# Kernel tuning notes

Hardware: AMD Instinct MI355X
Metric: run time of the kernel (lower is better)

The kernel has to match this reference:

```python
import jax, jax.numpy as jnp
import numpy as np

N, E = 50000, 800000
IN, HID, OUT = 128, 128, 64
H, ED = 4, 3
D = HID // H  # per-head dim = 32


def _w(key, shape):
    fan_in = shape[-1]
    return jax.random.normal(key, shape, dtype=jnp.float32) / np.sqrt(fan_in)


def setup_inputs() -> dict:
    key = jax.random.key(0)
    ks = jax.random.split(key, 32)
    inp = {
        "x": jax.random.normal(ks[0], (N, IN), dtype=jnp.float32),
        "edge_index": jax.random.randint(ks[1], (2, E), 0, N, dtype=jnp.int32),
        "edge_attr": jax.random.normal(ks[2], (E, ED), dtype=jnp.float32),
        # layer 1 TransformerConv (bias=False)
        "Wq1": _w(ks[3], (HID, IN)), "Wk1": _w(ks[4], (HID, IN)),
        "Wv1": _w(ks[5], (HID, IN)), "We1": _w(ks[6], (HID, ED)),
        "Ws1": _w(ks[7], (HID, IN)),
        # layer 1 MLP [HID,HID,HID]
        "M1a": _w(ks[8], (HID, HID)), "b1a": jnp.zeros((HID,), jnp.float32),
        "M1b": _w(ks[9], (HID, HID)), "b1b": jnp.zeros((HID,), jnp.float32),
        # layer 2 TransformerConv
        "Wq2": _w(ks[10], (HID, HID)), "Wk2": _w(ks[11], (HID, HID)),
        "Wv2": _w(ks[12], (HID, HID)), "We2": _w(ks[13], (HID, ED)),
        "Ws2": _w(ks[14], (HID, HID)),
        # layer 2 MLP
        "M2a": _w(ks[15], (HID, HID)), "b2a": jnp.zeros((HID,), jnp.float32),
        "M2b": _w(ks[16], (HID, HID)), "b2b": jnp.zeros((HID,), jnp.float32),
        # final MLP [HID,HID,OUT], plain_last=False
        "Wf1": _w(ks[17], (HID, HID)), "bf1": jnp.zeros((HID,), jnp.float32),
        "Wf2": _w(ks[18], (OUT, HID)), "bf2": jnp.zeros((OUT,), jnp.float32),
    }
    return inp


def _gelu(x):
    return jax.nn.gelu(x, approximate=True)


def _transformer_conv(x, src, dst, edge_attr, Wq, Wk, Wv, We, Ws, n_nodes):
    # PyG TransformerConv: x_j = x[src] (message source), x_i = x[dst] (target)
    q = (x @ Wq.T).reshape(n_nodes, H, D)
    e = (edge_attr @ We.T).reshape(-1, H, D)              # [E,H,D]
    k = (x @ Wk.T).reshape(n_nodes, H, D)[src] + e        # [E,H,D]
    v = (x @ Wv.T).reshape(n_nodes, H, D)[src] + e        # [E,H,D]
    alpha = jnp.einsum("ehd,ehd->eh", q[dst], k) / jnp.float32(np.sqrt(D))
    # segment softmax over incoming edges of each target node
    m = jax.ops.segment_max(alpha, dst, num_segments=n_nodes)  # [N,H]
    m = jnp.where(jnp.isfinite(m), m, 0.0)
    p = jnp.exp(alpha - m[dst])
    s = jax.ops.segment_sum(p, dst, num_segments=n_nodes)      # [N,H]
    a = p / jnp.maximum(s[dst], 1e-16)                         # [E,H]
    out = jax.ops.segment_sum(a[:, :, None] * v, dst, num_segments=n_nodes)
    out = out.reshape(n_nodes, H * D)
    # root_weight=True (default): skip connection through lin_skip (no bias)
    return out + x @ Ws.T


def _mlp2(x, Wa, ba, Wb, bb):
    # PyG MLP with plain_last=False: act after every linear, norm=None
    h = _gelu(x @ Wa.T + ba)
    return _gelu(h @ Wb.T + bb)


def reference(x, edge_index, edge_attr,
              Wq1, Wk1, Wv1, We1, Ws1, M1a, b1a, M1b, b1b,
              Wq2, Wk2, Wv2, We2, Ws2, M2a, b2a, M2b, b2b,
              Wf1, bf1, Wf2, bf2):
    n_nodes = x.shape[0]
    src, dst = edge_index[0], edge_index[1]
    h = _transformer_conv(x, src, dst, edge_attr, Wq1, Wk1, Wv1, We1, Ws1, n_nodes)
    h = h + _mlp2(h, M1a, b1a, M1b, b1b)
    h = _transformer_conv(h, src, dst, edge_attr, Wq2, Wk2, Wv2, We2, Ws2, n_nodes)
    h = h + _mlp2(h, M2a, b2a, M2b, b2b)
    return _mlp2(h, Wf1, bf1, Wf2, bf2)
```

## Files before the change

### kernel.cpp

```cpp
#include <hip/hip_runtime.h>
#include <hip/hip_bf16.h>
#include <math.h>

#define NN 50000
#define NE 800000
#define NPAD 50048
#define NB_SCAN 196

typedef unsigned short u16;
typedef unsigned int u32;
typedef __attribute__((ext_vector_type(8))) short short8;
typedef __attribute__((ext_vector_type(4))) float float4v;

__device__ __forceinline__ float us2f(u16 u) { return __uint_as_float(((unsigned)u) << 16); }
__device__ __forceinline__ float blo(u32 u) { return __uint_as_float(u << 16); }
__device__ __forceinline__ float bhi(u32 u) { return __uint_as_float(u & 0xffff0000u); }
__device__ __forceinline__ u16 f2us(float f) {
    unsigned x = __float_as_uint(f);
    return (u16)((x + 0x7FFFu + ((x >> 16) & 1u)) >> 16);
}
__device__ __forceinline__ float gelu_f(float x) {
    float p = x * x;
    float t = x * fmaf(p, 0.0713548162726f, 1.5957691216057308f);
    float e = __expf(-t);
    return x * __builtin_amdgcn_rcpf(1.0f + e);
}
__device__ __forceinline__ void lds_fence() {
    asm volatile("s_waitcnt lgkmcnt(0)" ::: "memory");
}

__device__ __forceinline__ float4v mfma4p(const u16* __restrict__ WP, int tile, int l,
                                          short8 a0, short8 a1, short8 a2, short8 a3) {
    const short8* wp = (const short8*)WP + (size_t)tile * 256 + l;
    short8 b0 = wp[0], b1 = wp[64], b2 = wp[128], b3 = wp[192];
    float4v acc = {0.f, 0.f, 0.f, 0.f};
    acc = __builtin_amdgcn_mfma_f32_16x16x32_bf16(a0, b0, acc, 0, 0, 0);
    acc = __builtin_amdgcn_mfma_f32_16x16x32_bf16(a1, b1, acc, 0, 0, 0);
    acc = __builtin_amdgcn_mfma_f32_16x16x32_bf16(a2, b2, acc, 0, 0, 0);
    acc = __builtin_amdgcn_mfma_f32_16x16x32_bf16(a3, b3, acc, 0, 0, 0);
    return acc;
}


__global__ void k_hist(const int* __restrict__ dstv, int* __restrict__ deg) {
    int e = blockIdx.x * blockDim.x + threadIdx.x;
    if (e < NE) atomicAdd(&deg[dstv[e]], 1);
}

__global__ __launch_bounds__(256) void k_scan1(const int* __restrict__ deg,
                                               int* __restrict__ rowstart,
                                               int* __restrict__ bsum) {
    __shared__ int wtot[4];
    int i = blockIdx.x * 256 + threadIdx.x;
    int lane = threadIdx.x & 63, w = threadIdx.x >> 6;
    int v = (i < NN) ? deg[i] : 0;
    int incl = v;
#pragma unroll
    for (int d = 1; d < 64; d <<= 1) {
        int tv = __shfl_up(incl, d);
        if (lane >= d) incl += tv;
    }
    if (lane == 63) wtot[w] = incl;
    __syncthreads();
    if (threadIdx.x == 0) {
        int s = 0;
#pragma unroll
        for (int j = 0; j < 4; ++j) { int t = wtot[j]; wtot[j] = s; s += t; }
        bsum[blockIdx.x] = s;
    }
    __syncthreads();
    if (i < NN) rowstart[i] = incl - v + wtot[w];
}

__global__ __launch_bounds__(256) void k_scan2(int* __restrict__ bsum) {
    __shared__ int wtot[4];
    int t = threadIdx.x;
    int lane = t & 63, w = t >> 6;
    int v = (t < NB_SCAN) ? bsum[t] : 0;
    int incl = v;
#pragma unroll
    for (int d = 1; d < 64; d <<= 1) {
        int tv = __shfl_up(incl, d);
        if (lane >= d) incl += tv;
    }
    if (lane == 63) wtot[w] = incl;
    __syncthreads();
    if (t == 0) {
        int s = 0;
#pragma unroll
        for (int j = 0; j < 4; ++j) { int tt = wtot[j]; wtot[j] = s; s += tt; }
    }
    __syncthreads();
    if (t < NB_SCAN) bsum[t] = incl - v + wtot[w];
}

__global__ void k_scan3(const int* __restrict__ bsum, int* __restrict__ rowstart,
                        int* __restrict__ cursor) {
    int i = blockIdx.x * 256 + threadIdx.x;
    if (i < NN) {
        int v = rowstart[i] + bsum[blockIdx.x];
        rowstart[i] = v;
        cursor[i] = v;
    }
    if (i == 0) rowstart[NN] = NE;
}

__global__ void k_scatter(const int* __restrict__ srcv, const int* __restrict__ dstv,
                          const float* __restrict__ eattr, int* __restrict__ cursor,
                          int4* __restrict__ rec) {
    int e = blockIdx.x * blockDim.x + threadIdx.x;
    if (e >= NE) return;
    int dst = dstv[e];
    int pos = atomicAdd(&cursor[dst], 1);
    int4 r;
    r.x = srcv[e];
    r.y = __float_as_int(eattr[e * 3 + 0]);
    r.z = __float_as_int(eattr[e * 3 + 1]);
    r.w = __float_as_int(eattr[e * 3 + 2]);
    rec[pos] = r;
}


struct CvtEnt { const float* s; u16* d; int n; };
struct CvtTab { CvtEnt e[14]; };
__global__ void k_cvt_w(CvtTab tab) {
    CvtEnt E = tab.e[blockIdx.x >> 3];
    int chunk = blockIdx.x & 7;
    int per = E.n >> 3;
    int lo = chunk * per, hi = lo + per;
    for (int o = lo + threadIdx.x; o < hi; o += blockDim.x) {
        int tile = o >> 11;
        int q = (o >> 9) & 3;
        int l = (o >> 3) & 63;
        int j = o & 7;
        int row = tile * 16 + (l & 15);
        int col = q * 32 + (l >> 4) * 8 + j;
        E.d[o] = f2us(E.s[row * 128 + col]);
    }
}

__global__ void k_prep_we(const float* __restrict__ We1, const float* __restrict__ We2,
                          float4* __restrict__ WeP1, float4* __restrict__ WeP2) {
    int t = threadIdx.x;
    if (t < 128) {
        WeP1[t] = make_float4(We1[t * 3], We1[t * 3 + 1], We1[t * 3 + 2], 0.f);
    } else {
        int c = t - 128;
        WeP2[c] = make_float4(We2[c * 3], We2[c * 3 + 1], We2[c * 3 + 2], 0.f);
    }
}


__device__ __forceinline__ void stage_plain(u16* buf, int kb, int m, int tt, float4v acc) {
#pragma unroll
    for (int r = 0; r < 4; ++r) buf[(kb * 4 + r) * 136 + tt * 16 + m] = f2us(acc[r]);
}
__device__ __forceinline__ void store128(const u16* buf, u16* dst, int r0w, int coff, int l) {
#pragma unroll
    for (int it = 0; it < 4; ++it) {
        int j = it * 64 + l;
        int row = j >> 4, col = (j & 15) * 8;
        *(uint4*)(dst + (size_t)(r0w + row) * 512 + coff + col) = *(const uint4*)&buf[row * 136 + col];
    }
}
__device__ __forceinline__ void read_frags(const u16* buf, int m, int kb,
                                           short8& f0, short8& f1, short8& f2, short8& f3) {
    const u16* p = buf + m * 136 + kb * 8;
    f0 = *(const short8*)(p);
    f1 = *(const short8*)(p + 32);
    f2 = *(const short8*)(p + 64);
    f3 = *(const short8*)(p + 96);
}

__device__ __forceinline__ void compute_g(const u16* buf, const float4* __restrict__ WeP,
                                          float4* __restrict__ G, int r0w, int m, int kb) {
    const u16* qr = buf + m * 136 + kb * 32;
    short8 qv0 = *(const short8*)(qr);
    short8 qv1 = *(const short8*)(qr + 8);
    short8 qv2 = *(const short8*)(qr + 16);
    short8 qv3 = *(const short8*)(qr + 24);
    const float4* wp = WeP + kb * 32;
    float g0 = 0.f, g1 = 0.f, g2 = 0.f;
    const short8* qs[4] = {&qv0, &qv1, &qv2, &qv3};
#pragma unroll
    for (int b = 0; b < 4; ++b) {
        const u16* qq = (const u16*)qs[b];
#pragma unroll
        for (int d = 0; d < 8; ++d) {
            float qvf = us2f(qq[d]);
            float4 wv = wp[b * 8 + d];
            g0 = fmaf(qvf, wv.x, g0);
            g1 = fmaf(qvf, wv.y, g1);
            g2 = fmaf(qvf, wv.z, g2);
        }
    }
    G[(size_t)(r0w + m) * 4 + kb] = make_float4(g0, g1, g2, 0.f);
}



__global__ __launch_bounds__(64, 4) void k_qkvs1(const float* __restrict__ Ain,
                                                 const u16* __restrict__ W,
                                                 const float4* __restrict__ WeP,
                                                 float4* __restrict__ G,
                                                 u16* __restrict__ QKVS) {
    __shared__ u16 my[16 * 136];
    int l = threadIdx.x;
    int m = l & 15, kb = l >> 4;
    int r0w = blockIdx.x * 16;

    short8 a0, a1, a2, a3;
    {
        const float* ap = Ain + (size_t)(r0w + m) * 128;
        bool ok = (r0w + m) < NN;
        short8* dsts[4] = {&a0, &a1, &a2, &a3};
#pragma unroll
        for (int i = 0; i < 4; ++i) {
            short8 r;
            if (ok) {
                const float* p = ap + (kb + i * 4) * 8;
                float4 f0 = *(const float4*)p;
                float4 f1 = *(const float4*)(p + 4);
                r[0]=(short)f2us(f0.x); r[1]=(short)f2us(f0.y); r[2]=(short)f2us(f0.z); r[3]=(short)f2us(f0.w);
                r[4]=(short)f2us(f1.x); r[5]=(short)f2us(f1.y); r[6]=(short)f2us(f1.z); r[7]=(short)f2us(f1.w);
            } else {
#pragma unroll
                for (int j = 0; j < 8; ++j) r[j] = 0;
            }
            *dsts[i] = r;
        }
    }

#pragma unroll
    for (int tt = 0; tt < 8; ++tt) stage_plain(my, kb, m, tt, mfma4p(W, tt, l, a0, a1, a2, a3));
    lds_fence();
    store128(my, QKVS, r0w, 0, l);
    compute_g(my, WeP, G, r0w, m, kb);
    lds_fence();
#pragma unroll
    for (int tt = 0; tt < 4; ++tt) {
        float4v acc = mfma4p(W, 8 + tt, l, a0, a1, a2, a3);
        int c = tt * 32 + 8 * (m >> 2) + (m & 3);
#pragma unroll
        for (int r = 0; r < 4; ++r) my[(kb * 4 + r) * 136 + c] = f2us(acc[r]);
    }
#pragma unroll
    for (int tt = 0; tt < 4; ++tt) {
        float4v acc = mfma4p(W, 16 + tt, l, a0, a1, a2, a3);
        int c = tt * 32 + 8 * (m >> 2) + (m & 3) + 4;
#pragma unroll
        for (int r = 0; r < 4; ++r) my[(kb * 4 + r) * 136 + c] = f2us(acc[r]);
    }
    lds_fence();
    store128(my, QKVS, r0w, 128, l);
    lds_fence();
#pragma unroll
    for (int tt = 0; tt < 4; ++tt) {
        float4v acc = mfma4p(W, 12 + tt, l, a0, a1, a2, a3);
        int c = tt * 32 + 8 * (m >> 2) + (m & 3);
#pragma unroll
        for (int r = 0; r < 4; ++r) my[(kb * 4 + r) * 136 + c] = f2us(acc[r]);
    }
#pragma unroll
    for (int tt = 0; tt < 4; ++tt) {
        float4v acc = mfma4p(W, 20 + tt, l, a0, a1, a2, a3);
        int c = tt * 32 + 8 * (m >> 2) + (m & 3) + 4;
#pragma unroll
        for (int r = 0; r < 4; ++r) my[(kb * 4 + r) * 136 + c] = f2us(acc[r]);
    }
    lds_fence();
    store128(my, QKVS, r0w, 256, l);
    lds_fence();
#pragma unroll
    for (int tt = 0; tt < 8; ++tt) stage_plain(my, kb, m, tt, mfma4p(W, 24 + tt, l, a0, a1, a2, a3));
    lds_fence();
    store128(my, QKVS, r0w, 384, l);
}


__global__ __launch_bounds__(64, 4) void k_mlp_qkvs(const u16* __restrict__ Ain,
                                                    const u16* __restrict__ Wm,
                                                    const float* __restrict__ bias1,
                                                    const float* __restrict__ bias2,
                                                    const u16* __restrict__ Wq,
                                                    const float4* __restrict__ WeP,
                                                    float4* __restrict__ G,
                                                    u16* __restrict__ QKVS) {
    __shared__ u16 sh[16 * 136];
    __shared__ u16 t1[16 * 136];
    int l = threadIdx.x;
    int m = l & 15, kb = l >> 4;
    int r0w = blockIdx.x * 16;

    const short8* arow = (const short8*)(Ain + (size_t)(r0w + m) * 128);
    short8 a0 = arow[kb], a1 = arow[kb + 4], a2 = arow[kb + 8], a3 = arow[kb + 12];
    {
        u16* p = sh + m * 136 + kb * 8;
        *(short8*)(p) = a0;
        *(short8*)(p + 32) = a1;
        *(short8*)(p + 64) = a2;
        *(short8*)(p + 96) = a3;
    }
#pragma unroll
    for (int tt = 0; tt < 8; ++tt) {
        float4v acc = mfma4p(Wm, tt, l, a0, a1, a2, a3);
        float bv = bias1[tt * 16 + m];
#pragma unroll
        for (int r = 0; r < 4; ++r)
            t1[(kb * 4 + r) * 136 + tt * 16 + m] = f2us(gelu_f(acc[r] + bv));
    }
    lds_fence();
    short8 c0, c1, c2, c3;
    read_frags(t1, m, kb, c0, c1, c2, c3);
#pragma unroll
    for (int tt = 0; tt < 8; ++tt) {
        float4v acc = mfma4p(Wm + 16384, tt, l, c0, c1, c2, c3);
        float bv = bias2[tt * 16 + m];
#pragma unroll
        for (int r = 0; r < 4; ++r) {
            int idx = (kb * 4 + r) * 136 + tt * 16 + m;
            sh[idx] = f2us(gelu_f(acc[r] + bv) + us2f(sh[idx]));
        }
    }
    lds_fence();
    short8 h0, h1, h2, h3;
    read_frags(sh, m, kb, h0, h1, h2, h3);

#pragma unroll
    for (int tt = 0; tt < 8; ++tt) stage_plain(t1, kb, m, tt, mfma4p(Wq, tt, l, h0, h1, h2, h3));
    lds_fence();
    store128(t1, QKVS, r0w, 0, l);
    compute_g(t1, WeP, G, r0w, m, kb);
    lds_fence();
#pragma unroll
    for (int tt = 0; tt < 4; ++tt) {
        float4v acc = mfma4p(Wq, 8 + tt, l, h0, h1, h2, h3);
        int c = tt * 32 + 8 * (m >> 2) + (m & 3);
#pragma unroll
        for (int r = 0; r < 4; ++r) t1[(kb * 4 + r) * 136 + c] = f2us(acc[r]);
    }
#pragma unroll
    for (int tt = 0; tt < 4; ++tt) {
        float4v acc = mfma4p(Wq, 16 + tt, l, h0, h1, h2, h3);
        int c = tt * 32 + 8 * (m >> 2) + (m & 3) + 4;
#pragma unroll
        for (int r = 0; r < 4; ++r) t1[(kb * 4 + r) * 136 + c] = f2us(acc[r]);
    }
    lds_fence();
    store128(t1, QKVS, r0w, 128, l);
    lds_fence();
#pragma unroll
    for (int tt = 0; tt < 4; ++tt) {
        float4v acc = mfma4p(Wq, 12 + tt, l, h0, h1, h2, h3);
        int c = tt * 32 + 8 * (m >> 2) + (m & 3);
#pragma unroll
        for (int r = 0; r < 4; ++r) t1[(kb * 4 + r) * 136 + c] = f2us(acc[r]);
    }
#pragma unroll
    for (int tt = 0; tt < 4; ++tt) {
        float4v acc = mfma4p(Wq, 20 + tt, l, h0, h1, h2, h3);
        int c = tt * 32 + 8 * (m >> 2) + (m & 3) + 4;
#pragma unroll
        for (int r = 0; r < 4; ++r) t1[(kb * 4 + r) * 136 + c] = f2us(acc[r]);
    }
    lds_fence();
    store128(t1, QKVS, r0w, 256, l);
    lds_fence();
#pragma unroll
    for (int tt = 0; tt < 8; ++tt) stage_plain(t1, kb, m, tt, mfma4p(Wq, 24 + tt, l, h0, h1, h2, h3));
    lds_fence();
    store128(t1, QKVS, r0w, 384, l);
}


__global__ __launch_bounds__(64, 4) void k_mlp_final(const u16* __restrict__ Ain,
                                                     const u16* __restrict__ Wm,
                                                     const float* __restrict__ bias1,
                                                     const float* __restrict__ bias2,
                                                     const u16* __restrict__ Wf,
                                                     const float* __restrict__ bf1,
                                                     const float* __restrict__ bf2,
                                                     float* __restrict__ outp) {
    __shared__ u16 sh[16 * 136];
    __shared__ u16 t1[16 * 136];
    int l = threadIdx.x;
    int m = l & 15, kb = l >> 4;
    int r0w = blockIdx.x * 16;

    const short8* arow = (const short8*)(Ain + (size_t)(r0w + m) * 128);
    short8 a0 = arow[kb], a1 = arow[kb + 4], a2 = arow[kb + 8], a3 = arow[kb + 12];
    {
        u16* p = sh + m * 136 + kb * 8;
        *(short8*)(p) = a0;
        *(short8*)(p + 32) = a1;
        *(short8*)(p + 64) = a2;
        *(short8*)(p + 96) = a3;
    }
#pragma unroll
    for (int tt = 0; tt < 8; ++tt) {
        float4v acc = mfma4p(Wm, tt, l, a0, a1, a2, a3);
        float bv = bias1[tt * 16 + m];
#pragma unroll
        for (int r = 0; r < 4; ++r)
            t1[(kb * 4 + r) * 136 + tt * 16 + m] = f2us(gelu_f(acc[r] + bv));
    }
    lds_fence();
    short8 c0, c1, c2, c3;
    read_frags(t1, m, kb, c0, c1, c2, c3);
#pragma unroll
    for (int tt = 0; tt < 8; ++tt) {
        float4v acc = mfma4p(Wm + 16384, tt, l, c0, c1, c2, c3);
        float bv = bias2[tt * 16 + m];
#pragma unroll
        for (int r = 0; r < 4; ++r) {
            int idx = (kb * 4 + r) * 136 + tt * 16 + m;
            sh[idx] = f2us(gelu_f(acc[r] + bv) + us2f(sh[idx]));
        }
    }
    lds_fence();
    short8 h0, h1, h2, h3;
    read_frags(sh, m, kb, h0, h1, h2, h3);
#pragma unroll
    for (int tt = 0; tt < 8; ++tt) {
        float4v acc = mfma4p(Wf, tt, l, h0, h1, h2, h3);
        float bv = bf1[tt * 16 + m];
#pragma unroll
        for (int r = 0; r < 4; ++r)
            t1[(kb * 4 + r) * 136 + tt * 16 + m] = f2us(gelu_f(acc[r] + bv));
    }
    lds_fence();
    short8 f0, f1, f2, f3;
    read_frags(t1, m, kb, f0, f1, f2, f3);
    lds_fence();
#pragma unroll
    for (int tt = 0; tt < 4; ++tt) {
        float4v acc = mfma4p(Wf + 16384, tt, l, f0, f1, f2, f3);
        float bv = bf2[tt * 16 + m];
#pragma unroll
        for (int r = 0; r < 4; ++r)
            t1[(kb * 4 + r) * 136 + tt * 16 + m] = f2us(gelu_f(acc[r] + bv));
    }
    lds_fence();
#pragma unroll
    for (int it = 0; it < 2; ++it) {
        int j = it * 64 + l;
        int row = j >> 3, col = (j & 7) * 8;
        int grow = r0w + row;
        if (grow < NN) {
            uint4 pk = *(const uint4*)&t1[row * 136 + col];
            const u16* pv = (const u16*)&pk;
            float* po = outp + (size_t)grow * 64 + col;
            float4 o0 = {us2f(pv[0]), us2f(pv[1]), us2f(pv[2]), us2f(pv[3])};
            float4 o1 = {us2f(pv[4]), us2f(pv[5]), us2f(pv[6]), us2f(pv[7])};
            *(float4*)po = o0;
            *(float4*)(po + 4) = o1;
        }
    }
}


__global__ __launch_bounds__(256) void k_conv(const int* __restrict__ rowstart,
                                              const int4* __restrict__ rec,
                                              const u16* __restrict__ qkvs,
                                              const float4* __restrict__ WeP,
                                              const float4* __restrict__ G,
                                              u16* __restrict__ out) {
    int n = blockIdx.x * 4 + (threadIdx.x >> 6);
    int l = threadIdx.x & 63;
    int quarter = l >> 4;
    int li = l & 15;
    int c0 = li * 8;
    const u16* qrow = qkvs + (size_t)n * 512;
    uint4 qu = *(const uint4*)(qrow + c0);
    const float SC = 0.17677669529663687f;
    float q0 = blo(qu.x) * SC, q1 = bhi(qu.x) * SC, q2 = blo(qu.y) * SC, q3 = bhi(qu.y) * SC;
    float q4 = blo(qu.z) * SC, q5 = bhi(qu.z) * SC, q6 = blo(qu.w) * SC, q7 = bhi(qu.w) * SC;
    float4 gg = G[(size_t)n * 4 + (li >> 2)];
    float g0 = gg.x * SC, g1 = gg.y * SC, g2 = gg.z * SC;

    int e0 = rowstart[n], e1 = rowstart[n + 1];
    int deg = e1 - e0;
    float ss = 0.f, S0 = 0.f, S1 = 0.f, S2 = 0.f;
    float o0 = 0.f, o1 = 0.f, o2 = 0.f, o3 = 0.f, o4 = 0.f, o5 = 0.f, o6 = 0.f, o7 = 0.f;

    if (deg > 0) {
        int iters = (deg + 3) >> 2;
        int eb = e0 + quarter;
        int elast = e1 - 1;
        int4 r0 = rec[min(eb, elast)];
        int4 r1 = rec[min(eb + 4, elast)];
        const u16* kvB = qkvs + 128 + (size_t)li * 16;
        uint4 kA = *(const uint4*)(kvB + (size_t)r0.x * 512);
        uint4 kB = *(const uint4*)(kvB + (size_t)r0.x * 512 + 8);
        for (int i = 0; i < iters; ++i) {
            int4 r2 = rec[min(eb + 4 * (i + 2), elast)];
            const u16* kp = kvB + (size_t)r1.x * 512;
            uint4 nA = *(const uint4*)(kp);
            uint4 nB = *(const uint4*)(kp + 8);
            float part = q0 * blo(kA.x) + q1 * bhi(kA.x) + q2 * blo(kA.y) + q3 * bhi(kA.y)
                       + q4 * blo(kB.x) + q5 * bhi(kB.x) + q6 * blo(kB.y) + q7 * bhi(kB.y);
            part += __shfl_xor(part, 1);
            part += __shfl_xor(part, 2);
            float ea0 = __int_as_float(r0.y), ea1 = __int_as_float(r0.z), ea2 = __int_as_float(r0.w);
            float alpha = fmaf(ea2, g2, fmaf(ea1, g1, fmaf(ea0, g0, part)));
            float p = __expf(fminf(alpha, 80.f));
            p = (eb + 4 * i < e1) ? p : 0.f;
            o0 = fmaf(p, blo(kA.z), o0);
            o1 = fmaf(p, bhi(kA.z), o1);
            o2 = fmaf(p, blo(kA.w), o2);
            o3 = fmaf(p, bhi(kA.w), o3);
            o4 = fmaf(p, blo(kB.z), o4);
            o5 = fmaf(p, bhi(kB.z), o5);
            o6 = fmaf(p, blo(kB.w), o6);
            o7 = fmaf(p, bhi(kB.w), o7);
            ss += p;
            S0 = fmaf(p, ea0, S0);
            S1 = fmaf(p, ea1, S1);
            S2 = fmaf(p, ea2, S2);
            r0 = r1; r1 = r2; kA = nA; kB = nB;
        }
    }
    o0 += __shfl_xor(o0, 16); o1 += __shfl_xor(o1, 16); o2 += __shfl_xor(o2, 16); o3 += __shfl_xor(o3, 16);
    o4 += __shfl_xor(o4, 16); o5 += __shfl_xor(o5, 16); o6 += __shfl_xor(o6, 16); o7 += __shfl_xor(o7, 16);
    ss += __shfl_xor(ss, 16); S0 += __shfl_xor(S0, 16); S1 += __shfl_xor(S1, 16); S2 += __shfl_xor(S2, 16);
    o0 += __shfl_xor(o0, 32); o1 += __shfl_xor(o1, 32); o2 += __shfl_xor(o2, 32); o3 += __shfl_xor(o3, 32);
    o4 += __shfl_xor(o4, 32); o5 += __shfl_xor(o5, 32); o6 += __shfl_xor(o6, 32); o7 += __shfl_xor(o7, 32);
    ss += __shfl_xor(ss, 32); S0 += __shfl_xor(S0, 32); S1 += __shfl_xor(S1, 32); S2 += __shfl_xor(S2, 32);

    if (quarter == 0) {
        float inv = __builtin_amdgcn_rcpf(fmaxf(ss, 1e-16f));
        float4 w0 = WeP[c0 + 0], w1 = WeP[c0 + 1], w2 = WeP[c0 + 2], w3 = WeP[c0 + 3];
        float4 w4 = WeP[c0 + 4], w5 = WeP[c0 + 5], w6 = WeP[c0 + 6], w7 = WeP[c0 + 7];
        o0 += w0.x * S0 + w0.y * S1 + w0.z * S2;
        o1 += w1.x * S0 + w1.y * S1 + w1.z * S2;
        o2 += w2.x * S0 + w2.y * S1 + w2.z * S2;
        o3 += w3.x * S0 + w3.y * S1 + w3.z * S2;
        o4 += w4.x * S0 + w4.y * S1 + w4.z * S2;
        o5 += w5.x * S0 + w5.y * S1 + w5.z * S2;
        o6 += w6.x * S0 + w6.y * S1 + w6.z * S2;
        o7 += w7.x * S0 + w7.y * S1 + w7.z * S2;
        uint4 su = *(const uint4*)(qrow + 384 + c0);
        float r0v = fmaf(o0, inv, blo(su.x));
        float r1v = fmaf(o1, inv, bhi(su.x));
        float r2v = fmaf(o2, inv, blo(su.y));
        float r3v = fmaf(o3, inv, bhi(su.y));
        float r4v = fmaf(o4, inv, blo(su.z));
        float r5v = fmaf(o5, inv, bhi(su.z));
        float r6v = fmaf(o6, inv, blo(su.w));
        float r7v = fmaf(o7, inv, bhi(su.w));
        uint4 ou;
        ou.x = (u32)f2us(r0v) | ((u32)f2us(r1v) << 16);
        ou.y = (u32)f2us(r2v) | ((u32)f2us(r3v) << 16);
        ou.z = (u32)f2us(r4v) | ((u32)f2us(r5v) << 16);
        ou.w = (u32)f2us(r6v) | ((u32)f2us(r7v) << 16);
        *(uint4*)(out + (size_t)n * 128 + c0) = ou;
    }
}


extern "C" void kernel_launch(void* const* d_in, const int* in_sizes, int n_in,
                              void* d_out, int out_size, void* d_ws, size_t ws_size,
                              hipStream_t stream) {
    const float* x = (const float*)d_in[0];
    const int* ei = (const int*)d_in[1];
    const float* eattr = (const float*)d_in[2];
    const float* Wq1 = (const float*)d_in[3];
    const float* Wk1 = (const float*)d_in[4];
    const float* Wv1 = (const float*)d_in[5];
    const float* We1 = (const float*)d_in[6];
    const float* Ws1 = (const float*)d_in[7];
    const float* M1a = (const float*)d_in[8];
    const float* b1a = (const float*)d_in[9];
    const float* M1b = (const float*)d_in[10];
    const float* b1b = (const float*)d_in[11];
    const float* Wq2 = (const float*)d_in[12];
    const float* Wk2 = (const float*)d_in[13];
    const float* Wv2 = (const float*)d_in[14];
    const float* We2 = (const float*)d_in[15];
    const float* Ws2 = (const float*)d_in[16];
    const float* M2a = (const float*)d_in[17];
    const float* b2a = (const float*)d_in[18];
    const float* M2b = (const float*)d_in[19];
    const float* b2b = (const float*)d_in[20];
    const float* Wf1 = (const float*)d_in[21];
    const float* bf1 = (const float*)d_in[22];
    const float* Wf2 = (const float*)d_in[23];
    const float* bf2 = (const float*)d_in[24];

    char* ws = (char*)d_ws;
    size_t off = 0;
    auto alloc = [&](size_t bytes) -> void* {
        void* p = ws + off;
        off = (off + bytes + 255) & ~(size_t)255;
        return p;
    };
    int* deg = (int*)alloc((size_t)NN * 4);
    int* rowstart = (int*)alloc((size_t)(NN + 1) * 4);
    int* cursor = (int*)alloc((size_t)NN * 4);
    int* bsum = (int*)alloc((size_t)NB_SCAN * 4);
    int4* rec = (int4*)alloc((size_t)NE * 16);
    u16* QKVS = (u16*)alloc((size_t)NPAD * 512 * 2);
    u16* Ha = (u16*)alloc((size_t)NPAD * 128 * 2);
    float4* G = (float4*)alloc((size_t)NPAD * 4 * 16);
    float4* WeP1 = (float4*)alloc(128 * 16);
    float4* WeP2 = (float4*)alloc(128 * 16);
    u16* WB[14];
    const int wsz[14] = {16384, 16384, 16384, 16384, 16384, 16384, 16384,
                         16384, 16384, 16384, 16384, 16384, 16384, 8192};
    for (int i = 0; i < 14; ++i) WB[i] = (u16*)alloc((size_t)wsz[i] * 2);

    const int* srcv = ei;
    const int* dstv = ei + NE;

    hipMemsetAsync(deg, 0, (size_t)NN * 4, stream);
    k_hist<<<(NE + 255) / 256, 256, 0, stream>>>(dstv, deg);
    k_scan1<<<NB_SCAN, 256, 0, stream>>>(deg, rowstart, bsum);
    k_scan2<<<1, 256, 0, stream>>>(bsum);
    k_scan3<<<NB_SCAN, 256, 0, stream>>>(bsum, rowstart, cursor);
    k_scatter<<<(NE + 255) / 256, 256, 0, stream>>>(srcv, dstv, eattr, cursor, rec);

    CvtTab tab;
    const float* wsrc[14] = {Wq1, Wk1, Wv1, Ws1, Wq2, Wk2, Wv2, Ws2,
                             M1a, M1b, M2a, M2b, Wf1, Wf2};
    for (int i = 0; i < 14; ++i) { tab.e[i].s = wsrc[i]; tab.e[i].d = WB[i]; tab.e[i].n = wsz[i]; }
    k_cvt_w<<<112, 256, 0, stream>>>(tab);
    k_prep_we<<<1, 256, 0, stream>>>(We1, We2, WeP1, WeP2);

    dim3 gg(NPAD / 16);
    dim3 gconv(NN / 4);

    k_qkvs1<<<gg, 64, 0, stream>>>(x, WB[0], WeP1, G, QKVS);
    k_conv<<<gconv, 256, 0, stream>>>(rowstart, rec, QKVS, WeP1, G, Ha);
    k_mlp_qkvs<<<gg, 64, 0, stream>>>(Ha, WB[8], b1a, b1b, WB[4], WeP2, G, QKVS);
    k_conv<<<gconv, 256, 0, stream>>>(rowstart, rec, QKVS, WeP2, G, Ha);
    k_mlp_final<<<gg, 64, 0, stream>>>(Ha, WB[10], b2a, b2b, WB[12], bf1, bf2, (float*)d_out);
}
```

Measured before the change: 412.1 us.

## Stage weight tiles in LDS shared by four waves per block in GEMM kernels

The three dense node-GEMM kernels now run four 16-row waves per 256-thread block. The waves cooperatively copy each 32 KB weight section into shared memory and then read MFMA B fragments from LDS, where each wave previously read the weights straight from global memory. This cuts global and L2 weight traffic by roughly a factor of four. In exchange it adds many __syncthreads barriers, serialises each load before its compute phase, and uses about 32 KB or more of LDS per block, which may lower occupancy.

Measured after the change: 437.1 us. 6.1% more time.

```diff
diff --git a/kernel.cpp b/kernel.cpp
--- a/kernel.cpp
+++ b/kernel.cpp
@@ -29,9 +29,9 @@
     asm volatile("s_waitcnt lgkmcnt(0)" ::: "memory");
 }
 
-__device__ __forceinline__ float4v mfma4p(const u16* __restrict__ WP, int tile, int l,
+__device__ __forceinline__ float4v mfma4l(const u16* sec, int t, int l,
                                           short8 a0, short8 a1, short8 a2, short8 a3) {
-    const short8* wp = (const short8*)WP + (size_t)tile * 256 + l;
+    const short8* wp = (const short8*)(sec + t * 2048) + l;
     short8 b0 = wp[0], b1 = wp[64], b2 = wp[128], b3 = wp[192];
     float4v acc = {0.f, 0.f, 0.f, 0.f};
     acc = __builtin_amdgcn_mfma_f32_16x16x32_bf16(a0, b0, acc, 0, 0, 0);
@@ -39,6 +39,29 @@
     acc = __builtin_amdgcn_mfma_f32_16x16x32_bf16(a2, b2, acc, 0, 0, 0);
     acc = __builtin_amdgcn_mfma_f32_16x16x32_bf16(a3, b3, acc, 0, 0, 0);
     return acc;
+}
+
+__device__ __forceinline__ void load_sec32(const u16* __restrict__ s0,
+                                           const u16* __restrict__ s1,
+                                           u16* secbuf, int w, int l) {
+    const u16* base = (w < 2) ? s0 : s1;
+    int off = (w & 1) * 8;
+    int dbase = (w < 2) ? 0 : 8192;
+#pragma unroll
+    for (int j = 0; j < 8; ++j) {
+        int ch = off + j;
+        uint4 v = *(const uint4*)(base + ch * 512 + l * 8);
+        *(uint4*)(secbuf + dbase + ch * 512 + l * 8) = v;
+    }
+}
+__device__ __forceinline__ void load_sec16(const u16* __restrict__ s0,
+                                           u16* secbuf, int w, int l) {
+#pragma unroll
+    for (int j = 0; j < 4; ++j) {
+        int ch = w * 4 + j;
+        uint4 v = *(const uint4*)(s0 + ch * 512 + l * 8);
+        *(uint4*)(secbuf + ch * 512 + l * 8) = v;
+    }
 }
 
 
@@ -175,16 +198,12 @@
 __device__ __forceinline__ void compute_g(const u16* buf, const float4* __restrict__ WeP,
                                           float4* __restrict__ G, int r0w, int m, int kb) {
     const u16* qr = buf + m * 136 + kb * 32;
-    short8 qv0 = *(const short8*)(qr);
-    short8 qv1 = *(const short8*)(qr + 8);
-    short8 qv2 = *(const short8*)(qr + 16);
-    short8 qv3 = *(const short8*)(qr + 24);
     const float4* wp = WeP + kb * 32;
     float g0 = 0.f, g1 = 0.f, g2 = 0.f;
-    const short8* qs[4] = {&qv0, &qv1, &qv2, &qv3};
 #pragma unroll
     for (int b = 0; b < 4; ++b) {
-        const u16* qq = (const u16*)qs[b];
+        short8 qv = *(const short8*)(qr + b * 8);
+        const u16* qq = (const u16*)&qv;
 #pragma unroll
         for (int d = 0; d < 8; ++d) {
             float qvf = us2f(qq[d]);
@@ -199,15 +218,17 @@
 
 
 
-__global__ __launch_bounds__(64, 4) void k_qkvs1(const float* __restrict__ Ain,
-                                                 const u16* __restrict__ W,
-                                                 const float4* __restrict__ WeP,
-                                                 float4* __restrict__ G,
-                                                 u16* __restrict__ QKVS) {
-    __shared__ u16 my[16 * 136];
-    int l = threadIdx.x;
-    int m = l & 15, kb = l >> 4;
-    int r0w = blockIdx.x * 16;
+__global__ __launch_bounds__(256) void k_qkvs1(const float* __restrict__ Ain,
+                                               const u16* __restrict__ W,
+                                               const float4* __restrict__ WeP,
+                                               float4* __restrict__ G,
+                                               u16* __restrict__ QKVS) {
+    __shared__ u16 secbuf[8 * 2048];
+    __shared__ u16 myb[4][16 * 136];
+    int tid = threadIdx.x;
+    int l = tid & 63, w = tid >> 6, m = l & 15, kb = l >> 4;
+    int r0w = blockIdx.x * 64 + w * 16;
+    u16* my = myb[w];
 
     short8 a0, a1, a2, a3;
     {
@@ -231,66 +252,77 @@
         }
     }
 
-#pragma unroll
-    for (int tt = 0; tt < 8; ++tt) stage_plain(my, kb, m, tt, mfma4p(W, tt, l, a0, a1, a2, a3));
+    load_sec32(W, W + 8192, secbuf, w, l);
+    __syncthreads();
+#pragma unroll
+    for (int tt = 0; tt < 8; ++tt) stage_plain(my, kb, m, tt, mfma4l(secbuf, tt, l, a0, a1, a2, a3));
     lds_fence();
     store128(my, QKVS, r0w, 0, l);
     compute_g(my, WeP, G, r0w, m, kb);
-    lds_fence();
-#pragma unroll
-    for (int tt = 0; tt < 4; ++tt) {
-        float4v acc = mfma4p(W, 8 + tt, l, a0, a1, a2, a3);
+    __syncthreads();
+    load_sec32(W + 8 * 2048, W + 16 * 2048, secbuf, w, l);
+    __syncthreads();
+#pragma unroll
+    for (int tt = 0; tt < 4; ++tt) {
+        float4v acc = mfma4l(secbuf, tt, l, a0, a1, a2, a3);
         int c = tt * 32 + 8 * (m >> 2) + (m & 3);
 #pragma unroll
         for (int r = 0; r < 4; ++r) my[(kb * 4 + r) * 136 + c] = f2us(acc[r]);
     }
 #pragma unroll
     for (int tt = 0; tt < 4; ++tt) {
-        float4v acc = mfma4p(W, 16 + tt, l, a0, a1, a2, a3);
+        float4v acc = mfma4l(secbuf, 4 + tt, l, a0, a1, a2, a3);
         int c = tt * 32 + 8 * (m >> 2) + (m & 3) + 4;
 #pragma unroll
         for (int r = 0; r < 4; ++r) my[(kb * 4 + r) * 136 + c] = f2us(acc[r]);
     }
     lds_fence();
     store128(my, QKVS, r0w, 128, l);
-    lds_fence();
-#pragma unroll
-    for (int tt = 0; tt < 4; ++tt) {
-        float4v acc = mfma4p(W, 12 + tt, l, a0, a1, a2, a3);
+    __syncthreads();
+    load_sec32(W + 12 * 2048, W + 20 * 2048, secbuf, w, l);
+    __syncthreads();
+#pragma unroll
+    for (int tt = 0; tt < 4; ++tt) {
+        float4v acc = mfma4l(secbuf, tt, l, a0, a1, a2, a3);
         int c = tt * 32 + 8 * (m >> 2) + (m & 3);
 #pragma unroll
         for (int r = 0; r < 4; ++r) my[(kb * 4 + r) * 136 + c] = f2us(acc[r]);
     }
 #pragma unroll
     for (int tt = 0; tt < 4; ++tt) {
-        float4v acc = mfma4p(W, 20 + tt, l, a0, a1, a2, a3);
+        float4v acc = mfma4l(secbuf, 4 + tt, l, a0, a1, a2, a3);
         int c = tt * 32 + 8 * (m >> 2) + (m & 3) + 4;
 #pragma unroll
         for (int r = 0; r < 4; ++r) my[(kb * 4 + r) * 136 + c] = f2us(acc[r]);
     }
     lds_fence();
     store128(my, QKVS, r0w, 256, l);
-    lds_fence();
-#pragma unroll
-    for (int tt = 0; tt < 8; ++tt) stage_plain(my, kb, m, tt, mfma4p(W, 24 + tt, l, a0, a1, a2, a3));
+    __syncthreads();
+    load_sec32(W + 24 * 2048, W + 28 * 2048, secbuf, w, l);
+    __syncthreads();
+#pragma unroll
+    for (int tt = 0; tt < 8; ++tt) stage_plain(my, kb, m, tt, mfma4l(secbuf, tt, l, a0, a1, a2, a3));
     lds_fence();
     store128(my, QKVS, r0w, 384, l);
 }
 
 
-__global__ __launch_bounds__(64, 4) void k_mlp_qkvs(const u16* __restrict__ Ain,
-                                                    const u16* __restrict__ Wm,
-                                                    const float* __restrict__ bias1,
-                                                    const float* __restrict__ bias2,
-                                                    const u16* __restrict__ Wq,
-                                                    const float4* __restrict__ WeP,
-                                                    float4* __restrict__ G,
-                                                    u16* __restrict__ QKVS) {
-    __shared__ u16 sh[16 * 136];
-    __shared__ u16 t1[16 * 136];
-    int l = threadIdx.x;
-    int m = l & 15, kb = l >> 4;
-    int r0w = blockIdx.x * 16;
+__global__ __launch_bounds__(256) void k_mlp_qkvs(const u16* __restrict__ Ain,
+                                                  const u16* __restrict__ Wm,
+                                                  const float* __restrict__ bias1,
+                                                  const float* __restrict__ bias2,
+                                                  const u16* __restrict__ Wq,
+                                                  const float4* __restrict__ WeP,
+                                                  float4* __restrict__ G,
+                                                  u16* __restrict__ QKVS) {
+    __shared__ u16 secbuf[8 * 2048];
+    __shared__ u16 shb[4][16 * 136];
+    __shared__ u16 t1b[4][16 * 136];
+    int tid = threadIdx.x;
+    int l = tid & 63, w = tid >> 6, m = l & 15, kb = l >> 4;
+    int r0w = blockIdx.x * 64 + w * 16;
+    u16* sh = shb[w];
+    u16* t1 = t1b[w];
 
     const short8* arow = (const short8*)(Ain + (size_t)(r0w + m) * 128);
     short8 a0 = arow[kb], a1 = arow[kb + 4], a2 = arow[kb + 8], a3 = arow[kb + 12];
@@ -301,9 +333,11 @@
         *(short8*)(p + 64) = a2;
         *(short8*)(p + 96) = a3;
     }
+    load_sec32(Wm, Wm + 8192, secbuf, w, l);
+    __syncthreads();
 #pragma unroll
     for (int tt = 0; tt < 8; ++tt) {
-        float4v acc = mfma4p(Wm, tt, l, a0, a1, a2, a3);
+        float4v acc = mfma4l(secbuf, tt, l, a0, a1, a2, a3);
         float bv = bias1[tt * 16 + m];
 #pragma unroll
         for (int r = 0; r < 4; ++r)
@@ -312,9 +346,12 @@
     lds_fence();
     short8 c0, c1, c2, c3;
     read_frags(t1, m, kb, c0, c1, c2, c3);
+    __syncthreads();
+    load_sec32(Wm + 16384, Wm + 16384 + 8192, secbuf, w, l);
+    __syncthreads();
 #pragma unroll
     for (int tt = 0; tt < 8; ++tt) {
-        float4v acc = mfma4p(Wm + 16384, tt, l, c0, c1, c2, c3);
+        float4v acc = mfma4l(secbuf, tt, l, c0, c1, c2, c3);
         float bv = bias2[tt * 16 + m];
 #pragma unroll
         for (int r = 0; r < 4; ++r) {
@@ -325,67 +362,78 @@
     lds_fence();
     short8 h0, h1, h2, h3;
     read_frags(sh, m, kb, h0, h1, h2, h3);
-
-#pragma unroll
-    for (int tt = 0; tt < 8; ++tt) stage_plain(t1, kb, m, tt, mfma4p(Wq, tt, l, h0, h1, h2, h3));
+    __syncthreads();
+    load_sec32(Wq, Wq + 8192, secbuf, w, l);
+    __syncthreads();
+#pragma unroll
+    for (int tt = 0; tt < 8; ++tt) stage_plain(t1, kb, m, tt, mfma4l(secbuf, tt, l, h0, h1, h2, h3));
     lds_fence();
     store128(t1, QKVS, r0w, 0, l);
     compute_g(t1, WeP, G, r0w, m, kb);
-    lds_fence();
-#pragma unroll
-    for (int tt = 0; tt < 4; ++tt) {
-        float4v acc = mfma4p(Wq, 8 + tt, l, h0, h1, h2, h3);
+    __syncthreads();
+    load_sec32(Wq + 8 * 2048, Wq + 16 * 2048, secbuf, w, l);
+    __syncthreads();
+#pragma unroll
+    for (int tt = 0; tt < 4; ++tt) {
+        float4v acc = mfma4l(secbuf, tt, l, h0, h1, h2, h3);
         int c = tt * 32 + 8 * (m >> 2) + (m & 3);
 #pragma unroll
         for (int r = 0; r < 4; ++r) t1[(kb * 4 + r) * 136 + c] = f2us(acc[r]);
     }
 #pragma unroll
     for (int tt = 0; tt < 4; ++tt) {
-        float4v acc = mfma4p(Wq, 16 + tt, l, h0, h1, h2, h3);
+        float4v acc = mfma4l(secbuf, 4 + tt, l, h0, h1, h2, h3);
         int c = tt * 32 + 8 * (m >> 2) + (m & 3) + 4;
 #pragma unroll
         for (int r = 0; r < 4; ++r) t1[(kb * 4 + r) * 136 + c] = f2us(acc[r]);
     }
     lds_fence();
     store128(t1, QKVS, r0w, 128, l);
-    lds_fence();
-#pragma unroll
-    for (int tt = 0; tt < 4; ++tt) {
-        float4v acc = mfma4p(Wq, 12 + tt, l, h0, h1, h2, h3);
+    __syncthreads();
+    load_sec32(Wq + 12 * 2048, Wq + 20 * 2048, secbuf, w, l);
+    __syncthreads();
+#pragma unroll
+    for (int tt = 0; tt < 4; ++tt) {
+        float4v acc = mfma4l(secbuf, tt, l, h0, h1, h2, h3);
         int c = tt * 32 + 8 * (m >> 2) + (m & 3);
 #pragma unroll
         for (int r = 0; r < 4; ++r) t1[(kb * 4 + r) * 136 + c] = f2us(acc[r]);
     }
 #pragma unroll
     for (int tt = 0; tt < 4; ++tt) {
-        float4v acc = mfma4p(Wq, 20 + tt, l, h0, h1, h2, h3);
+        float4v acc = mfma4l(secbuf, 4 + tt, l, h0, h1, h2, h3);
         int c = tt * 32 + 8 * (m >> 2) + (m & 3) + 4;
 #pragma unroll
         for (int r = 0; r < 4; ++r) t1[(kb * 4 + r) * 136 + c] = f2us(acc[r]);
     }
     lds_fence();
     store128(t1, QKVS, r0w, 256, l);
-    lds_fence();
-#pragma unroll
-    for (int tt = 0; tt < 8; ++tt) stage_plain(t1, kb, m, tt, mfma4p(Wq, 24 + tt, l, h0, h1, h2, h3));
+    __syncthreads();
+    load_sec32(Wq + 24 * 2048, Wq + 28 * 2048, secbuf, w, l);
+    __syncthreads();
+#pragma unroll
+    for (int tt = 0; tt < 8; ++tt) stage_plain(t1, kb, m, tt, mfma4l(secbuf, tt, l, h0, h1, h2, h3));
     lds_fence();
     store128(t1, QKVS, r0w, 384, l);
 }
 
 
-__global__ __launch_bounds__(64, 4) void k_mlp_final(const u16* __restrict__ Ain,
-                                                     const u16* __restrict__ Wm,
-                                                     const float* __restrict__ bias1,
-                                                     const float* __restrict__ bias2,
-                                                     const u16* __restrict__ Wf,
-                                                     const float* __restrict__ bf1,
-                                                     const float* __restrict__ bf2,
-                                                     float* __restrict__ outp) {
-    __shared__ u16 sh[16 * 136];
-    __shared__ u16 t1[16 * 136];
-    int l = threadIdx.x;
-    int m = l & 15, kb = l >> 4;
-    int r0w = blockIdx.x * 16;
+__global__ __launch_bounds__(256) void k_mlp_final(const u16* __restrict__ Ain,
+                                                   const u16* __restrict__ Wm,
+                                                   const float* __restrict__ bias1,
+                                                   const float* __restrict__ bias2,
+                                                   const u16* __restrict__ Wf,
+                                                   const float* __restrict__ bf1,
+                                                   const float* __restrict__ bf2,
+                                                   float* __restrict__ outp) {
+    __shared__ u16 secbuf[8 * 2048];
+    __shared__ u16 shb[4][16 * 136];
+    __shared__ u16 t1b[4][16 * 136];
+    int tid = threadIdx.x;
+    int l = tid & 63, w = tid >> 6, m = l & 15, kb = l >> 4;
+    int r0w = blockIdx.x * 64 + w * 16;
+    u16* sh = shb[w];
+    u16* t1 = t1b[w];
 
     const short8* arow = (const short8*)(Ain + (size_t)(r0w + m) * 128);
     short8 a0 = arow[kb], a1 = arow[kb + 4], a2 = arow[kb + 8], a3 = arow[kb + 12];
@@ -396,9 +444,11 @@
         *(short8*)(p + 64) = a2;
         *(short8*)(p + 96) = a3;
     }
+    load_sec32(Wm, Wm + 8192, secbuf, w, l);
+    __syncthreads();
 #pragma unroll
     for (int tt = 0; tt < 8; ++tt) {
-        float4v acc = mfma4p(Wm, tt, l, a0, a1, a2, a3);
+        float4v acc = mfma4l(secbuf, tt, l, a0, a1, a2, a3);
         float bv = bias1[tt * 16 + m];
 #pragma unroll
         for (int r = 0; r < 4; ++r)
@@ -407,9 +457,12 @@
     lds_fence();
     short8 c0, c1, c2, c3;
     read_frags(t1, m, kb, c0, c1, c2, c3);
+    __syncthreads();
+    load_sec32(Wm + 16384, Wm + 16384 + 8192, secbuf, w, l);
+    __syncthreads();
 #pragma unroll
     for (int tt = 0; tt < 8; ++tt) {
-        float4v acc = mfma4p(Wm + 16384, tt, l, c0, c1, c2, c3);
+        float4v acc = mfma4l(secbuf, tt, l, c0, c1, c2, c3);
         float bv = bias2[tt * 16 + m];
 #pragma unroll
         for (int r = 0; r < 4; ++r) {
@@ -420,9 +473,12 @@
     lds_fence();
     short8 h0, h1, h2, h3;
     read_frags(sh, m, kb, h0, h1, h2, h3);
+    __syncthreads();
+    load_sec32(Wf, Wf + 8192, secbuf, w, l);
+    __syncthreads();
 #pragma unroll
     for (int tt = 0; tt < 8; ++tt) {
-        float4v acc = mfma4p(Wf, tt, l, h0, h1, h2, h3);
+        float4v acc = mfma4l(secbuf, tt, l, h0, h1, h2, h3);
         float bv = bf1[tt * 16 + m];
 #pragma unroll
         for (int r = 0; r < 4; ++r)
@@ -431,10 +487,12 @@
     lds_fence();
     short8 f0, f1, f2, f3;
     read_frags(t1, m, kb, f0, f1, f2, f3);
-    lds_fence();
-#pragma unroll
-    for (int tt = 0; tt < 4; ++tt) {
-        float4v acc = mfma4p(Wf + 16384, tt, l, f0, f1, f2, f3);
+    __syncthreads();
+    load_sec16(Wf + 16384, secbuf, w, l);
+    __syncthreads();
+#pragma unroll
+    for (int tt = 0; tt < 4; ++tt) {
+        float4v acc = mfma4l(secbuf, tt, l, f0, f1, f2, f3);
         float bv = bf2[tt * 16 + m];
 #pragma unroll
         for (int r = 0; r < 4; ++r)
@@ -626,12 +684,12 @@
     k_cvt_w<<<112, 256, 0, stream>>>(tab);
     k_prep_we<<<1, 256, 0, stream>>>(We1, We2, WeP1, WeP2);
 
-    dim3 gg(NPAD / 16);
+    dim3 grd(NPAD / 64);
     dim3 gconv(NN / 4);
 
-    k_qkvs1<<<gg, 64, 0, stream>>>(x, WB[0], WeP1, G, QKVS);
+    k_qkvs1<<<grd, 256, 0, stream>>>(x, WB[0], WeP1, G, QKVS);
     k_conv<<<gconv, 256, 0, stream>>>(rowstart, rec, QKVS, WeP1, G, Ha);
-    k_mlp_qkvs<<<gg, 64, 0, stream>>>(Ha, WB[8], b1a, b1b, WB[4], WeP2, G, QKVS);
+    k_mlp_qkvs<<<grd, 256, 0, stream>>>(Ha, WB[8], b1a, b1b, WB[4], WeP2, G, QKVS);
     k_conv<<<gconv, 256, 0, stream>>>(rowstart, rec, QKVS, WeP2, G, Ha);
-    k_mlp_final<<<gg, 64, 0, stream>>>(Ha, WB[10], b2a, b2b, WB[12], bf1, bf2, (float*)d_out);
-}
+    k_mlp_final<<<grd, 256, 0, stream>>>(Ha, WB[10], b2a, b2b, WB[12], bf1, bf2, (float*)d_out);
+}
```
